# Optimization experiments

Hardware: AMD Instinct MI355X
Metric: run time of the kernel (lower is better)

Reference implementation:

```python
import jax, jax.numpy as jnp
import numpy as np

# Grid / window constants (match init_kwargs)
GX, GY, GZ = 120, 120, 8          # grid_size (x, y, z)
WX, WY, WZ = 8, 8, 2              # window_shape
T = WX * WY * WZ                  # 128 slots per window
C = 48                            # channels after conv_input
H = 8                             # nhead
HD = C // H                       # head dim = 6
FF = 256                          # dim_feedforward
N = 80000                         # occupied voxels
NW = (GX // WX) * (GY // WY) * (GZ // WZ)  # 900 windows (batch_size=1)


def _ln(x, g, b, eps=1e-5):
    mu = jnp.mean(x, -1, keepdims=True)
    var = jnp.mean((x - mu) ** 2, -1, keepdims=True)
    return (x - mu) * jax.lax.rsqrt(var + eps) * g + b


def setup_inputs() -> dict:
    key = jax.random.key(0)
    ks = jax.random.split(key, 16)
    # unique voxel coords (no duplicate (window, slot) pairs)
    rng = np.random.default_rng(0)
    lin = rng.choice(GX * GY * GZ, N, replace=False)
    z = lin // (GX * GY)
    rem = lin % (GX * GY)
    y = rem // GX
    x = rem % GX
    coords = np.stack([np.zeros(N, np.int32), z.astype(np.int32), y.astype(np.int32), x.astype(np.int32)], 1)
    s = 0.02
    inp = {
        "voxel_features": jax.random.normal(ks[0], (N, C), jnp.float32),
        "voxel_coords": jnp.asarray(coords, jnp.int32),
        "Wq": jax.random.normal(ks[1], (C, C)) * s, "bq": jnp.zeros((C,)),
        "Wk": jax.random.normal(ks[2], (C, C)) * s, "bk": jnp.zeros((C,)),
        "Wv": jax.random.normal(ks[3], (C, C)) * s, "bv": jnp.zeros((C,)),
        "Wo": jax.random.normal(ks[4], (C, C)) * s, "bo": jnp.zeros((C,)),
        "ln1_g": jnp.ones((C,)), "ln1_b": jnp.zeros((C,)),
        "W1": jax.random.normal(ks[5], (C, FF)) * s, "b1": jnp.zeros((FF,)),
        "W2": jax.random.normal(ks[6], (FF, C)) * s, "b2": jnp.zeros((C,)),
        "ln2_g": jnp.ones((C,)), "ln2_b": jnp.zeros((C,)),
    }
    return inp


def reference(voxel_features, voxel_coords, Wq, bq, Wk, bk, Wv, bv, Wo, bo,
              ln1_g, ln1_b, W1, b1, W2, b2, ln2_g, ln2_b):
    b = voxel_coords[:, 0]
    z, y, x = voxel_coords[:, 1], voxel_coords[:, 2], voxel_coords[:, 3]
    # window id and in-window slot (unique per voxel)
    win = ((b * (GZ // WZ) + z // WZ) * (GY // WY) + y // WY) * (GX // WX) + x // WX
    slot = (z % WZ) * (WY * WX) + (y % WY) * WX + (x % WX)
    # scatter to padded window buffers  [NW, T, C]
    buf = jnp.zeros((NW, T, C), voxel_features.dtype).at[win, slot].set(voxel_features)
    valid = jnp.zeros((NW, T), bool).at[win, slot].set(True)
    # multi-head self-attention within each window
    q = (buf @ Wq + bq).reshape(NW, T, H, HD)
    k = (buf @ Wk + bk).reshape(NW, T, H, HD)
    v = (buf @ Wv + bv).reshape(NW, T, H, HD)
    scores = jnp.einsum("nqhd,nkhd->nhqk", q, k) / jnp.sqrt(jnp.asarray(HD, buf.dtype))
    scores = jnp.where(valid[:, None, None, :], scores, jnp.asarray(-1e9, buf.dtype))
    attn = jax.nn.softmax(scores, axis=-1)
    ctx = jnp.einsum("nhqk,nkhd->nqhd", attn, v).reshape(NW, T, C)
    ctx = ctx @ Wo + bo
    h = _ln(buf + ctx, ln1_g, ln1_b)                  # post-norm residual 1
    ff = jax.nn.relu(h @ W1 + b1) @ W2 + b2           # FFN
    h = _ln(h + ff, ln2_g, ln2_b)                     # post-norm residual 2
    # scatter back to sparse voxel list  [N, C]
    return h[win, slot]
```

## Files before the change

### kernel.cpp

```cpp
#include <hip/hip_runtime.h>
#include <hip/hip_bf16.h>

constexpr int kGX = 120, kGY = 120, kGZ = 8;
constexpr int kWX = 8, kWY = 8, kWZ = 2;
constexpr int kT  = 128;
constexpr int kC  = 48;
constexpr int kFF = 256;
constexpr int kNW = (kGX/kWX)*(kGY/kWY)*(kGZ/kWZ);
constexpr int kN  = 80000;

constexpr int BQ = 9216,  BK = 9264,  BV = 9312,  BO = 9360;
constexpr int G1 = 9408,  B1L = 9456, G2 = 9504,  B2L = 9552;
constexpr int B1F = 21888;
constexpr int B2F = 34432;
constexpr int WTOT = 34480;

constexpr size_t alup(size_t x) { return ((x + 255) / 256) * 256; }
constexpr size_t SLOT_OFF = alup((size_t)WTOT * 4);
constexpr size_t WQT_OFF  = alup(SLOT_OFF + (size_t)kNW * kT * 4);
constexpr size_t WKT_OFF  = WQT_OFF + 4608;
constexpr size_t WVT_OFF  = WKT_OFF + 4608;
constexpr size_t WOT_OFF  = WVT_OFF + 4608;
constexpr size_t W1TB_OFF = alup(WOT_OFF + 4608);
constexpr size_t W2TB_OFF = alup(W1TB_OFF + (size_t)kFF * kC * 2);
constexpr size_t P0       = alup(W2TB_OFF + (size_t)kC * kFF * 2);
constexpr size_t RSZ      = (size_t)kN * kC * 2;
constexpr size_t QS_OFF   = P0;
constexpr size_t KB_OFF   = P0 + RSZ;
constexpr size_t VB_OFF   = P0 + 2*RSZ;
constexpr size_t CTX_OFF  = P0 + 3*RSZ;
constexpr size_t H_OFF    = alup(P0 + 4*RSZ);

typedef short  bf16x8 __attribute__((ext_vector_type(8)));
typedef float  f32x4  __attribute__((ext_vector_type(4)));
typedef float  f32x2  __attribute__((ext_vector_type(2)));

#if __has_builtin(__builtin_amdgcn_exp2f)
#define EXP2F(x) __builtin_amdgcn_exp2f(x)
#else
#define EXP2F(x) exp2f(x)
#endif

__device__ __forceinline__ float bf2f(unsigned int bits16) {
  return __uint_as_float(bits16 << 16);
}
__device__ __forceinline__ unsigned short f2bf(float f) {
  unsigned int u = __float_as_uint(f);
  u += 0x7fffu + ((u >> 16) & 1u);
  return (unsigned short)(u >> 16);
}
__device__ __forceinline__ f32x2 mkf2(float a, float b) {
  f32x2 r; r.x = a; r.y = b; return r;
}
__device__ __forceinline__ int get_isbf(const unsigned int* g1) {
  return (*g1 != 0x3F800000u) ? 1 : 0;
}

struct ConvArgs {
  const void* src[16];
  void*       dst[16];
  int rows[16];
  int cols[16];
  int obf[16];
};

__global__ void k_prep(ConvArgs a, const unsigned int* __restrict__ g1,
                       const int* __restrict__ coords, int* __restrict__ sm) {
  if (blockIdx.x < 16) {
    const int isbf = get_isbf(g1);
    const int s = blockIdx.x;
    const int R = a.rows[s], C = a.cols[s];
    const int n = R * C;
    const int ob = a.obf[s];
    for (int i = threadIdx.x; i < n; i += blockDim.x) {
      float v = isbf ? bf2f(((const unsigned short*)a.src[s])[i])
                     : ((const float*)a.src[s])[i];
      int oi = i;
      if (C > 1) { int r = i / C, c = i - r * C; oi = c * R + r; }
      if (ob) ((unsigned short*)a.dst[s])[oi] = f2bf(v);
      else    ((float*)a.dst[s])[oi] = v;
    }
  } else {
    int v = (blockIdx.x - 16) * blockDim.x + threadIdx.x;
    if (v >= kN) return;
    int z = coords[v*4 + 1], y = coords[v*4 + 2], x = coords[v*4 + 3];
    int win  = ((z/kWZ) * (kGY/kWY) + y/kWY) * (kGX/kWX) + x/kWX;
    int slot = (z%kWZ) * (kWY*kWX) + (y%kWY) * kWX + (x%kWX);
    sm[win*kT + slot] = v;
  }
}

__global__ __attribute__((amdgpu_waves_per_eu(2, 4))) __launch_bounds__(256)
void k_qkv3(const void* __restrict__ feats_raw,
            const unsigned int* __restrict__ g1,
            const unsigned short* __restrict__ wqt,
            const unsigned short* __restrict__ wkt,
            const unsigned short* __restrict__ wvt,
            const float* __restrict__ w,
            unsigned short* __restrict__ Qs,
            unsigned short* __restrict__ Kb,
            unsigned short* __restrict__ Vb)
{
  __shared__ unsigned short At[128*72];
  __shared__ unsigned short Bt[3][48*72];

  const int isbf = get_isbf(g1);
  const int tid = threadIdx.x, bm = blockIdx.x;

  if (isbf) {
    const uint4* asrc = (const uint4*)((const unsigned short*)feats_raw +
                                       (size_t)bm * 128 * kC);
    #pragma unroll
    for (int i = 0; i < 3; ++i) {
      int cid = tid + 256*i;
      int row = cid / 6, ch = cid - row*6;
      *(uint4*)((char*)At + row*144 + ch*16) = asrc[row*6 + ch];
    }
  } else {
    const float4* asrc = (const float4*)((const float*)feats_raw +
                                         (size_t)bm * 128 * kC);
    #pragma unroll
    for (int i = 0; i < 3; ++i) {
      int cid = tid + 256*i;
      int row = cid / 6, ch = cid - row*6;
      float4 f0 = asrc[row*12 + ch*2], f1 = asrc[row*12 + ch*2 + 1];
      uint4 o;
      o.x = (unsigned int)f2bf(f0.x) | ((unsigned int)f2bf(f0.y) << 16);
      o.y = (unsigned int)f2bf(f0.z) | ((unsigned int)f2bf(f0.w) << 16);
      o.z = (unsigned int)f2bf(f1.x) | ((unsigned int)f2bf(f1.y) << 16);
      o.w = (unsigned int)f2bf(f1.z) | ((unsigned int)f2bf(f1.w) << 16);
      *(uint4*)((char*)At + row*144 + ch*16) = o;
    }
  }
  {
    int row = tid >> 1, ch = 6 + (tid & 1);
    *(uint4*)((char*)At + row*144 + ch*16) = make_uint4(0,0,0,0);
  }
  #pragma unroll
  for (int y = 0; y < 3; ++y) {
    const uint4* bsrc = (const uint4*)((y == 0) ? wqt : (y == 1) ? wkt : wvt);
    #pragma unroll
    for (int i = 0; i < 2; ++i) {
      int cid = tid + 256*i;
      if (cid < 288) {
        int row = cid / 6, ch = cid - row*6;
        *(uint4*)((char*)Bt[y] + row*144 + ch*16) = bsrc[row*6 + ch];
      }
    }
    if (tid < 96) {
      int row = tid >> 1, ch = 6 + (tid & 1);
      *(uint4*)((char*)Bt[y] + row*144 + ch*16) = make_uint4(0,0,0,0);
    }
  }
  __syncthreads();

  const int lane = tid & 63, wv = tid >> 6;
  const int moff = wv * 32;
  const int lr = lane & 15, lc = lane >> 4;

  #pragma unroll
  for (int y = 0; y < 3; ++y) {
    unsigned short* dst = (y == 0) ? Qs : (y == 1) ? Kb : Vb;
    const float* bias = w + ((y == 0) ? BQ : (y == 1) ? BK : BV);
    const float scl = (y == 0) ? 0.5889777931f : 1.0f;

    f32x4 acc[2][3] = {};
    #pragma unroll
    for (int ks = 0; ks < 2; ++ks) {
      bf16x8 a[2], b[3];
      #pragma unroll
      for (int m = 0; m < 2; ++m)
        a[m] = *(const bf16x8*)((const char*)At +
                (moff + m*16 + lr)*144 + lc*16 + ks*64);
      #pragma unroll
      for (int n = 0; n < 3; ++n)
        b[n] = *(const bf16x8*)((const char*)Bt[y] +
                (n*16 + lr)*144 + lc*16 + ks*64);
      #pragma unroll
      for (int m = 0; m < 2; ++m)
        #pragma unroll
        for (int n = 0; n < 3; ++n)
          acc[m][n] = __builtin_amdgcn_mfma_f32_16x16x32_bf16(
                          a[m], b[n], acc[m][n], 0, 0, 0);
    }
    #pragma unroll
    for (int n = 0; n < 3; ++n) {
      const int col = n*16 + lr;
      const float bv = bias[col];
      #pragma unroll
      for (int m = 0; m < 2; ++m) {
        const int row0 = bm*128 + moff + m*16 + lc*4;
        #pragma unroll
        for (int r = 0; r < 4; ++r)
          dst[(size_t)(row0 + r) * kC + col] = f2bf((acc[m][n][r] + bv) * scl);
      }
    }
  }
}

#define ATTN_KEY(KK, ACC, LP) {                                               \
    const float4* kp_ = (const float4*)(KfF + (size_t)(KK)*48 + q*12);        \
    const float4* vp_ = (const float4*)(VfF + (size_t)(KK)*48 + q*12);        \
    float4 k0_ = kp_[0], k1_ = kp_[1], k2_ = kp_[2];                          \
    f32x2 p0_ = qp[0] * mkf2(k0_.x, k0_.y);                                   \
    p0_ += qp[1] * mkf2(k0_.z, k0_.w);                                        \
    p0_ += qp[2] * mkf2(k1_.x, k1_.y);                                        \
    f32x2 p1_ = qp[3] * mkf2(k1_.z, k1_.w);                                   \
    p1_ += qp[4] * mkf2(k2_.x, k2_.y);                                        \
    p1_ += qp[5] * mkf2(k2_.z, k2_.w);                                        \
    float w0_ = EXP2F(p0_.x + p0_.y);                                         \
    float w1_ = EXP2F(p1_.x + p1_.y);                                         \
    float4 v0_ = vp_[0], v1_ = vp_[1], v2_ = vp_[2];                          \
    LP += mkf2(w0_, w1_);                                                     \
    f32x2 w0p_ = mkf2(w0_, w0_), w1p_ = mkf2(w1_, w1_);                       \
    ACC[0] += w0p_ * mkf2(v0_.x, v0_.y);                                      \
    ACC[1] += w0p_ * mkf2(v0_.z, v0_.w);                                      \
    ACC[2] += w0p_ * mkf2(v1_.x, v1_.y);                                      \
    ACC[3] += w1p_ * mkf2(v1_.z, v1_.w);                                      \
    ACC[4] += w1p_ * mkf2(v2_.x, v2_.y);                                      \
    ACC[5] += w1p_ * mkf2(v2_.z, v2_.w);                                      \
  }

__global__ __attribute__((amdgpu_waves_per_eu(2, 6))) __launch_bounds__(512)
void k_attn2f(const unsigned short* __restrict__ Qs,
              const unsigned short* __restrict__ Kb,
              const unsigned short* __restrict__ Vb,
              const int* __restrict__ sm,
              unsigned short* __restrict__ ctxb)
{
  __shared__ __align__(16) float KfF[kT*kC];
  __shared__ __align__(16) float VfF[kT*kC];
  __shared__ int posmap[kT];
  __shared__ unsigned long long wmask[2];

  const int win = blockIdx.x;
  const int tid = threadIdx.x;
  const int q   = tid >> 7;
  const int t   = tid & 127;
  const int vid = sm[win*kT + t];
  const bool valid = vid >= 0;

  unsigned long long bm = __ballot(valid);
  if (tid < 128 && (tid & 63) == 0) wmask[tid >> 6] = bm;
  __syncthreads();

  const int cnt0 = __popcll(wmask[0]);
  const int nk   = cnt0 + __popcll(wmask[1]);
  if (tid < 128) {
    int pos = -1;
    if (valid) {
      unsigned long long lanemask = (1ull << (t & 63)) - 1ull;
      pos = ((t >> 6) ? cnt0 : 0) + __popcll(wmask[t >> 6] & lanemask);
    }
    posmap[t] = pos;
  }
  __syncthreads();

  #pragma unroll
  for (int i = 0; i < 3; ++i) {
    int cid = tid + 512*i;
    int mat = cid / 768;
    int r   = cid - mat*768;
    int slot = r / 6, ch = r - slot*6;
    int p = posmap[slot];
    if (p >= 0) {
      int svid = sm[win*kT + slot];
      const unsigned short* src = mat ? Vb : Kb;
      uint4 u = *(const uint4*)(src + (size_t)svid * kC + ch*8);
      float* d = (mat ? VfF : KfF) + p*48 + ch*8;
      float4 f0, f1;
      f0.x = bf2f(u.x & 0xffffu); f0.y = bf2f(u.x >> 16);
      f0.z = bf2f(u.y & 0xffffu); f0.w = bf2f(u.y >> 16);
      f1.x = bf2f(u.z & 0xffffu); f1.y = bf2f(u.z >> 16);
      f1.z = bf2f(u.w & 0xffffu); f1.w = bf2f(u.w >> 16);
      *(float4*)d = f0;
      *(float4*)(d + 4) = f1;
    }
  }
  __syncthreads();

  f32x2 qp[6];
  #pragma unroll
  for (int j = 0; j < 6; ++j) qp[j] = mkf2(0.f, 0.f);
  if (valid) {
    const unsigned short* qptr = Qs + (size_t)vid * kC + q*12;
    uint2 q0 = *(const uint2*)(qptr);
    uint2 q1 = *(const uint2*)(qptr + 4);
    uint2 q2 = *(const uint2*)(qptr + 8);
    unsigned int qw[6] = {q0.x, q0.y, q1.x, q1.y, q2.x, q2.y};
    #pragma unroll
    for (int j = 0; j < 6; ++j)
      qp[j] = mkf2(bf2f(qw[j] & 0xffffu), bf2f(qw[j] >> 16));
  }

  f32x2 accA[6], accB[6];
  f32x2 lA = mkf2(0.f, 0.f), lB = mkf2(0.f, 0.f);
  #pragma unroll
  for (int j = 0; j < 6; ++j) { accA[j] = mkf2(0.f, 0.f); accB[j] = mkf2(0.f, 0.f); }

  int i = 0;
  for (; i + 2 <= nk; i += 2) {
    ATTN_KEY(i,     accA, lA);
    ATTN_KEY(i + 1, accB, lB);
  }
  if (i < nk) {
    ATTN_KEY(i, accA, lA);
  }
  lA += lB;
  #pragma unroll
  for (int j = 0; j < 6; ++j) accA[j] += accB[j];

  if (valid) {
    float i0 = (lA.x > 0.f) ? (1.f / lA.x) : 0.f;
    float i1 = (lA.y > 0.f) ? (1.f / lA.y) : 0.f;
    unsigned int pw[6];
    #pragma unroll
    for (int j = 0; j < 6; ++j) {
      float sc = (j < 3) ? i0 : i1;
      pw[j] = (unsigned int)f2bf(accA[j].x * sc) |
              ((unsigned int)f2bf(accA[j].y * sc) << 16);
    }
    unsigned short* cp = ctxb + (size_t)vid * kC + q*12;
    *(uint2*)(cp)     = make_uint2(pw[0], pw[1]);
    *(uint2*)(cp + 4) = make_uint2(pw[2], pw[3]);
    *(uint2*)(cp + 8) = make_uint2(pw[4], pw[5]);
  }
}

__global__ __attribute__((amdgpu_waves_per_eu(2, 4))) __launch_bounds__(256)
void k_woln1(const unsigned short* __restrict__ ctxb,
             const unsigned short* __restrict__ wot,
             const void* __restrict__ feats_raw,
             const unsigned int* __restrict__ g1,
             const float* __restrict__ w,
             unsigned short* __restrict__ hbuf)
{
  __shared__ unsigned short At[128*72];
  __shared__ unsigned short Bt[48*72];
  __shared__ float Cf[128][49];

  const int isbf = get_isbf(g1);
  const int tid = threadIdx.x, bm = blockIdx.x;

  const uint4* asrc = (const uint4*)(ctxb + (size_t)bm * 128 * kC);
  #pragma unroll
  for (int i = 0; i < 3; ++i) {
    int cid = tid + 256*i;
    int row = cid / 6, ch = cid - row*6;
    *(uint4*)((char*)At + row*144 + ch*16) = asrc[row*6 + ch];
  }
  {
    int row = tid >> 1, ch = 6 + (tid & 1);
    *(uint4*)((char*)At + row*144 + ch*16) = make_uint4(0,0,0,0);
  }
  {
    const uint4* bsrc = (const uint4*)wot;
    #pragma unroll
    for (int i = 0; i < 2; ++i) {
      int cid = tid + 256*i;
      if (cid < 288) {
        int row = cid / 6, ch = cid - row*6;
        *(uint4*)((char*)Bt + row*144 + ch*16) = bsrc[row*6 + ch];
      }
    }
    if (tid < 96) {
      int row = tid >> 1, ch = 6 + (tid & 1);
      *(uint4*)((char*)Bt + row*144 + ch*16) = make_uint4(0,0,0,0);
    }
  }
  __syncthreads();

  const int lane = tid & 63, wv = tid >> 6;
  const int moff = wv * 32;
  const int lr = lane & 15, lc = lane >> 4;

  f32x4 acc[2][3] = {};
  #pragma unroll
  for (int ks = 0; ks < 2; ++ks) {
    bf16x8 a[2], b[3];
    #pragma unroll
    for (int m = 0; m < 2; ++m)
      a[m] = *(const bf16x8*)((const char*)At +
              (moff + m*16 + lr)*144 + lc*16 + ks*64);
    #pragma unroll
    for (int n = 0; n < 3; ++n)
      b[n] = *(const bf16x8*)((const char*)Bt +
              (n*16 + lr)*144 + lc*16 + ks*64);
    #pragma unroll
    for (int m = 0; m < 2; ++m)
      #pragma unroll
      for (int n = 0; n < 3; ++n)
        acc[m][n] = __builtin_amdgcn_mfma_f32_16x16x32_bf16(
                        a[m], b[n], acc[m][n], 0, 0, 0);
  }

  #pragma unroll
  for (int n = 0; n < 3; ++n) {
    const int col = n*16 + lr;
    const float bo = w[BO + col];
    #pragma unroll
    for (int m = 0; m < 2; ++m) {
      const int row0 = moff + m*16 + lc*4;
      #pragma unroll
      for (int r = 0; r < 4; ++r)
        Cf[row0 + r][col] = acc[m][n][r] + bo;
    }
  }
  __syncthreads();

  if (tid < 128) {
    const size_t gvox = (size_t)bm * 128 + tid;
    float xrow[kC];
    if (isbf) {
      const uint4* xp = (const uint4*)((const unsigned short*)feats_raw +
                                       gvox * kC);
      #pragma unroll
      for (int i = 0; i < 6; ++i) {
        uint4 u = xp[i];
        unsigned int uu[4] = {u.x, u.y, u.z, u.w};
        #pragma unroll
        for (int j = 0; j < 4; ++j) {
          xrow[i*8 + j*2 + 0] = bf2f(uu[j] & 0xffffu);
          xrow[i*8 + j*2 + 1] = bf2f(uu[j] >> 16);
        }
      }
    } else {
      const float4* xp = (const float4*)((const float*)feats_raw + gvox * kC);
      #pragma unroll
      for (int i = 0; i < 12; ++i) {
        float4 u = xp[i];
        xrow[i*4+0] = u.x; xrow[i*4+1] = u.y;
        xrow[i*4+2] = u.z; xrow[i*4+3] = u.w;
      }
    }
    float val[kC];
    float mu = 0.f;
    #pragma unroll
    for (int c = 0; c < kC; ++c) {
      float v = Cf[tid][c] + xrow[c];
      val[c] = v;
      mu += v;
    }
    mu *= (1.f / kC);
    float var = 0.f;
    #pragma unroll
    for (int c = 0; c < kC; ++c) { float d = val[c] - mu; var += d * d; }
    var *= (1.f / kC);
    float rs = rsqrtf(var + 1e-5f);

    unsigned int pk[kC/2];
    #pragma unroll
    for (int cp = 0; cp < kC/2; ++cp) {
      float h0 = (val[2*cp]   - mu) * rs * w[G1 + 2*cp]   + w[B1L + 2*cp];
      float h1 = (val[2*cp+1] - mu) * rs * w[G1 + 2*cp+1] + w[B1L + 2*cp+1];
      pk[cp] = (unsigned int)f2bf(h0) | ((unsigned int)f2bf(h1) << 16);
    }
    uint4* op = (uint4*)(hbuf + gvox * kC);
    #pragma unroll
    for (int i = 0; i < 6; ++i)
      op[i] = make_uint4(pk[i*4+0], pk[i*4+1], pk[i*4+2], pk[i*4+3]);
  }
}

__global__ __attribute__((amdgpu_waves_per_eu(2, 2))) __launch_bounds__(256)
void k_ffln(const unsigned short* __restrict__ hb,
            const unsigned short* __restrict__ w1tb,
            const unsigned short* __restrict__ w2tb,
            const float* __restrict__ w,
            void* __restrict__ out_raw,
            const unsigned int* __restrict__ g1)
{
  __shared__ __align__(16) char L[71424];
  unsigned short* W2t = (unsigned short*)(L + 18432);
  unsigned short* Bt  = (unsigned short*)(L + 43776);
  unsigned short* Ut  = (unsigned short*)(L + 52992);
  float* Cf = (float*)(L + 43776);

  const int isbf = get_isbf(g1);
  const int tid = threadIdx.x, bm = blockIdx.x;

  const uint4* hsrc = (const uint4*)(hb + (size_t)bm * 128 * kC);
  #pragma unroll
  for (int i = 0; i < 3; ++i) {
    int cid = tid + 256*i;
    int row = cid / 6, ch = cid - row*6;
    *(uint4*)(L + row*144 + ch*16) = hsrc[row*6 + ch];
  }
  {
    int row = tid >> 1, ch = 6 + (tid & 1);
    *(uint4*)(L + row*144 + ch*16) = make_uint4(0,0,0,0);
  }
  {
    const uint4* wsrc = (const uint4*)w2tb;
    #pragma unroll
    for (int i = 0; i < 6; ++i) {
      int cid = tid + 256*i;
      int row = cid >> 5, ch = cid & 31;
      *(uint4*)((char*)W2t + row*528 + ch*16) = wsrc[row*32 + ch];
    }
  }

  const int lane = tid & 63, wv = tid >> 6;
  const int moff = wv * 32;
  const int lr = lane & 15, lc = lane >> 4;

  f32x4 acc2[2][3] = {};

  for (int qn = 0; qn < 4; ++qn) {
    __syncthreads();
    {
      const uint4* bsrc = (const uint4*)(w1tb + (size_t)qn * 64 * kC);
      #pragma unroll
      for (int i = 0; i < 2; ++i) {
        int cid = tid + 256*i;
        if (cid < 384) {
          int row = cid / 6, ch = cid - row*6;
          *(uint4*)((char*)Bt + row*144 + ch*16) = bsrc[row*6 + ch];
        }
      }
      if (tid < 128) {
        int row = tid >> 1, ch = 6 + (tid & 1);
        *(uint4*)((char*)Bt + row*144 + ch*16) = make_uint4(0,0,0,0);
      }
    }
    __syncthreads();

    f32x4 acc1[2][4] = {};
    #pragma unroll
    for (int ks = 0; ks < 2; ++ks) {
      bf16x8 a[2], b[4];
      #pragma unroll
      for (int m = 0; m < 2; ++m)
        a[m] = *(const bf16x8*)(L + (moff + m*16 + lr)*144 + lc*16 + ks*64);
      #pragma unroll
      for (int n = 0; n < 4; ++n)
        b[n] = *(const bf16x8*)((const char*)Bt +
                (n*16 + lr)*144 + lc*16 + ks*64);
      #pragma unroll
      for (int m = 0; m < 2; ++m)
        #pragma unroll
        for (int n = 0; n < 4; ++n)
          acc1[m][n] = __builtin_amdgcn_mfma_f32_16x16x32_bf16(
                           a[m], b[n], acc1[m][n], 0, 0, 0);
    }

    #pragma unroll
    for (int n = 0; n < 4; ++n) {
      const float bias = w[B1F + qn*64 + n*16 + lr];
      #pragma unroll
      for (int m = 0; m < 2; ++m) {
        #pragma unroll
        for (int r = 0; r < 4; ++r) {
          float v = fmaxf(acc1[m][n][r] + bias, 0.f);
          Ut[(moff + m*16 + lc*4 + r)*72 + n*16 + lr] = f2bf(v);
        }
      }
    }

    #pragma unroll
    for (int ks = 0; ks < 2; ++ks) {
      bf16x8 a[2], b[3];
      #pragma unroll
      for (int m = 0; m < 2; ++m)
        a[m] = *(const bf16x8*)((const char*)Ut +
                (moff + m*16 + lr)*144 + lc*16 + ks*64);
      #pragma unroll
      for (int n = 0; n < 3; ++n)
        b[n] = *(const bf16x8*)((const char*)W2t +
                (n*16 + lr)*528 + qn*128 + ks*64 + lc*16);
      #pragma unroll
      for (int m = 0; m < 2; ++m)
        #pragma unroll
        for (int n = 0; n < 3; ++n)
          acc2[m][n] = __builtin_amdgcn_mfma_f32_16x16x32_bf16(
                           a[m], b[n], acc2[m][n], 0, 0, 0);
    }
  }

  __syncthreads();

  #pragma unroll
  for (int n = 0; n < 3; ++n) {
    const int col = n*16 + lr;
    const float b2v = w[B2F + col];
    #pragma unroll
    for (int m = 0; m < 2; ++m) {
      const int row0 = moff + m*16 + lc*4;
      #pragma unroll
      for (int r = 0; r < 4; ++r)
        Cf[(row0 + r)*49 + col] = acc2[m][n][r] + b2v;
    }
  }
  __syncthreads();

  if (tid < 128) {
    const size_t gvox = (size_t)bm * 128 + tid;
    const uint4* hp = (const uint4*)(hb + gvox * kC);
    float val[kC];
    float mu = 0.f;
    #pragma unroll
    for (int i = 0; i < 6; ++i) {
      uint4 u = hp[i];
      unsigned int uu[4] = {u.x, u.y, u.z, u.w};
      #pragma unroll
      for (int j = 0; j < 4; ++j) {
        float v0 = Cf[tid*49 + i*8 + j*2 + 0] + bf2f(uu[j] & 0xffffu);
        float v1 = Cf[tid*49 + i*8 + j*2 + 1] + bf2f(uu[j] >> 16);
        val[i*8 + j*2 + 0] = v0;
        val[i*8 + j*2 + 1] = v1;
        mu += v0 + v1;
      }
    }
    mu *= (1.f / kC);
    float var = 0.f;
    #pragma unroll
    for (int c = 0; c < kC; ++c) { float d = val[c] - mu; var += d * d; }
    var *= (1.f / kC);
    float rs = rsqrtf(var + 1e-5f);

    float ov[kC];
    #pragma unroll
    for (int c = 0; c < kC; ++c)
      ov[c] = (val[c] - mu) * rs * w[G2 + c] + w[B2L + c];

    if (isbf) {
      unsigned int pk[kC/2];
      #pragma unroll
      for (int c = 0; c < kC; c += 2)
        pk[c/2] = (unsigned int)f2bf(ov[c]) | ((unsigned int)f2bf(ov[c+1]) << 16);
      uint4* op = (uint4*)((unsigned short*)out_raw + gvox * kC);
      #pragma unroll
      for (int i = 0; i < 6; ++i)
        op[i] = make_uint4(pk[i*4+0], pk[i*4+1], pk[i*4+2], pk[i*4+3]);
    } else {
      float4* op = (float4*)((float*)out_raw + gvox * kC);
      #pragma unroll
      for (int i = 0; i < 12; ++i)
        op[i] = make_float4(ov[i*4+0], ov[i*4+1], ov[i*4+2], ov[i*4+3]);
    }
  }
}

extern "C" void kernel_launch(void* const* d_in, const int* in_sizes, int n_in,
                              void* d_out, int out_size, void* d_ws, size_t ws_size,
                              hipStream_t stream) {
  const void* feats = d_in[0];
  const int* coords = (const int*)d_in[1];
  const unsigned int* g1 = (const unsigned int*)d_in[10];
  char* ws = (char*)d_ws;
  float* wbuf = (float*)d_ws;
  int* sm   = (int*)(ws + SLOT_OFF);
  unsigned short* wqt  = (unsigned short*)(ws + WQT_OFF);
  unsigned short* wkt  = (unsigned short*)(ws + WKT_OFF);
  unsigned short* wvt  = (unsigned short*)(ws + WVT_OFF);
  unsigned short* wot  = (unsigned short*)(ws + WOT_OFF);
  unsigned short* w1tb = (unsigned short*)(ws + W1TB_OFF);
  unsigned short* w2tb = (unsigned short*)(ws + W2TB_OFF);
  unsigned short* Qs   = (unsigned short*)(ws + QS_OFF);
  unsigned short* Kb   = (unsigned short*)(ws + KB_OFF);
  unsigned short* Vb   = (unsigned short*)(ws + VB_OFF);
  unsigned short* ctxb = (unsigned short*)(ws + CTX_OFF);
  unsigned short* hbuf = (unsigned short*)(ws + H_OFF);

  ConvArgs ca;
  const int srcIdx[16] = {2,4,6,8, 3,5,7,9, 10,11,16,17, 12,13,14,15};
  void* dsts[16] = {
    wqt, wkt, wvt, wot,
    wbuf+BQ, wbuf+BK, wbuf+BV, wbuf+BO,
    wbuf+G1, wbuf+B1L, wbuf+G2, wbuf+B2L,
    w1tb, wbuf+B1F, w2tb, wbuf+B2F };
  const int rows[16] = {48,48,48,48, 48,48,48,48, 48,48,48,48, 48,256,256,48};
  const int cols[16] = {48,48,48,48, 1,1,1,1, 1,1,1,1, 256,1,48,1};
  const int obfs[16] = {1,1,1,1, 0,0,0,0, 0,0,0,0, 1,0,1,0};
  for (int i = 0; i < 16; ++i) {
    ca.src[i]  = d_in[srcIdx[i]];
    ca.dst[i]  = dsts[i];
    ca.rows[i] = rows[i];
    ca.cols[i] = cols[i];
    ca.obf[i]  = obfs[i];
  }

  hipMemsetAsync(sm, 0xFF, (size_t)kNW * kT * 4, stream);
  hipLaunchKernelGGL(k_prep, dim3(16 + (kN + 255)/256), dim3(256), 0, stream,
                     ca, g1, coords, sm);
  hipLaunchKernelGGL(k_qkv3, dim3(kN/128), dim3(256), 0, stream,
                     feats, g1, wqt, wkt, wvt, wbuf, Qs, Kb, Vb);
  hipLaunchKernelGGL(k_attn2f, dim3(kNW), dim3(512), 0, stream,
                     Qs, Kb, Vb, sm, ctxb);
  hipLaunchKernelGGL(k_woln1, dim3(kN/128), dim3(256), 0, stream,
                     ctxb, wot, feats, g1, wbuf, hbuf);
  hipLaunchKernelGGL(k_ffln, dim3(kN/128), dim3(256), 0, stream,
                     hbuf, w1tb, w2tb, wbuf, d_out, g1);
}
```

Measured before the change: 117.4 us.

## Process two queries per thread in attention to reuse K/V shared loads

The attention kernel now launches 256 threads per window instead of 512, and each thread handles two query slots (lane and lane+64) for a quarter of the heads. Each K/V row read from shared memory feeds both queries, halving LDS traffic per unit of work. In exchange it uses more registers per thread, runs fewer threads per block, and drops the two-key unrolling, which may cut latency hiding.

```diff
diff --git a/kernel.cpp b/kernel.cpp
--- a/kernel.cpp
+++ b/kernel.cpp
@@ -198,31 +198,8 @@
   }
 }
 
-#define ATTN_KEY(KK, ACC, LP) {                                               \
-    const float4* kp_ = (const float4*)(KfF + (size_t)(KK)*48 + q*12);        \
-    const float4* vp_ = (const float4*)(VfF + (size_t)(KK)*48 + q*12);        \
-    float4 k0_ = kp_[0], k1_ = kp_[1], k2_ = kp_[2];                          \
-    f32x2 p0_ = qp[0] * mkf2(k0_.x, k0_.y);                                   \
-    p0_ += qp[1] * mkf2(k0_.z, k0_.w);                                        \
-    p0_ += qp[2] * mkf2(k1_.x, k1_.y);                                        \
-    f32x2 p1_ = qp[3] * mkf2(k1_.z, k1_.w);                                   \
-    p1_ += qp[4] * mkf2(k2_.x, k2_.y);                                        \
-    p1_ += qp[5] * mkf2(k2_.z, k2_.w);                                        \
-    float w0_ = EXP2F(p0_.x + p0_.y);                                         \
-    float w1_ = EXP2F(p1_.x + p1_.y);                                         \
-    float4 v0_ = vp_[0], v1_ = vp_[1], v2_ = vp_[2];                          \
-    LP += mkf2(w0_, w1_);                                                     \
-    f32x2 w0p_ = mkf2(w0_, w0_), w1p_ = mkf2(w1_, w1_);                       \
-    ACC[0] += w0p_ * mkf2(v0_.x, v0_.y);                                      \
-    ACC[1] += w0p_ * mkf2(v0_.z, v0_.w);                                      \
-    ACC[2] += w0p_ * mkf2(v1_.x, v1_.y);                                      \
-    ACC[3] += w1p_ * mkf2(v1_.z, v1_.w);                                      \
-    ACC[4] += w1p_ * mkf2(v2_.x, v2_.y);                                      \
-    ACC[5] += w1p_ * mkf2(v2_.z, v2_.w);                                      \
-  }
-
-__global__ __attribute__((amdgpu_waves_per_eu(2, 6))) __launch_bounds__(512)
-void k_attn2f(const unsigned short* __restrict__ Qs,
+__global__ __attribute__((amdgpu_waves_per_eu(2, 4))) __launch_bounds__(256)
+void k_attn2h(const unsigned short* __restrict__ Qs,
               const unsigned short* __restrict__ Kb,
               const unsigned short* __restrict__ Vb,
               const int* __restrict__ sm,
@@ -233,32 +210,33 @@
   __shared__ int posmap[kT];
   __shared__ unsigned long long wmask[2];
 
-  const int win = blockIdx.x;
-  const int tid = threadIdx.x;
-  const int q   = tid >> 7;
-  const int t   = tid & 127;
-  const int vid = sm[win*kT + t];
-  const bool valid = vid >= 0;
-
-  unsigned long long bm = __ballot(valid);
-  if (tid < 128 && (tid & 63) == 0) wmask[tid >> 6] = bm;
+  const int win  = blockIdx.x;
+  const int tid  = threadIdx.x;
+  const int q    = tid >> 6;
+  const int lane = tid & 63;
+
+  if (tid < 128) {
+    bool val = sm[win*kT + tid] >= 0;
+    unsigned long long bm = __ballot(val);
+    if ((tid & 63) == 0) wmask[tid >> 6] = bm;
+  }
   __syncthreads();
 
   const int cnt0 = __popcll(wmask[0]);
   const int nk   = cnt0 + __popcll(wmask[1]);
   if (tid < 128) {
     int pos = -1;
-    if (valid) {
-      unsigned long long lanemask = (1ull << (t & 63)) - 1ull;
-      pos = ((t >> 6) ? cnt0 : 0) + __popcll(wmask[t >> 6] & lanemask);
-    }
-    posmap[t] = pos;
+    if (sm[win*kT + tid] >= 0) {
+      unsigned long long lanemask = (1ull << (tid & 63)) - 1ull;
+      pos = ((tid >> 6) ? cnt0 : 0) + __popcll(wmask[tid >> 6] & lanemask);
+    }
+    posmap[tid] = pos;
   }
   __syncthreads();
 
   #pragma unroll
-  for (int i = 0; i < 3; ++i) {
-    int cid = tid + 512*i;
+  for (int i = 0; i < 6; ++i) {
+    int cid = tid + 256*i;
     int mat = cid / 768;
     int r   = cid - mat*768;
     int slot = r / 6, ch = r - slot*6;
@@ -279,18 +257,32 @@
   }
   __syncthreads();
 
-  f32x2 qp[6];
-  #pragma unroll
-  for (int j = 0; j < 6; ++j) qp[j] = mkf2(0.f, 0.f);
-  if (valid) {
-    const unsigned short* qptr = Qs + (size_t)vid * kC + q*12;
+  const int vidA = sm[win*kT + lane];
+  const int vidB = sm[win*kT + 64 + lane];
+  const bool validA = vidA >= 0, validB = vidB >= 0;
+
+  f32x2 qpA[6], qpB[6];
+  #pragma unroll
+  for (int j = 0; j < 6; ++j) { qpA[j] = mkf2(0.f, 0.f); qpB[j] = mkf2(0.f, 0.f); }
+  if (validA) {
+    const unsigned short* qptr = Qs + (size_t)vidA * kC + q*12;
     uint2 q0 = *(const uint2*)(qptr);
     uint2 q1 = *(const uint2*)(qptr + 4);
     uint2 q2 = *(const uint2*)(qptr + 8);
     unsigned int qw[6] = {q0.x, q0.y, q1.x, q1.y, q2.x, q2.y};
     #pragma unroll
     for (int j = 0; j < 6; ++j)
-      qp[j] = mkf2(bf2f(qw[j] & 0xffffu), bf2f(qw[j] >> 16));
+      qpA[j] = mkf2(bf2f(qw[j] & 0xffffu), bf2f(qw[j] >> 16));
+  }
+  if (validB) {
+    const unsigned short* qptr = Qs + (size_t)vidB * kC + q*12;
+    uint2 q0 = *(const uint2*)(qptr);
+    uint2 q1 = *(const uint2*)(qptr + 4);
+    uint2 q2 = *(const uint2*)(qptr + 8);
+    unsigned int qw[6] = {q0.x, q0.y, q1.x, q1.y, q2.x, q2.y};
+    #pragma unroll
+    for (int j = 0; j < 6; ++j)
+      qpB[j] = mkf2(bf2f(qw[j] & 0xffffu), bf2f(qw[j] >> 16));
   }
 
   f32x2 accA[6], accB[6];
@@ -298,19 +290,49 @@
   #pragma unroll
   for (int j = 0; j < 6; ++j) { accA[j] = mkf2(0.f, 0.f); accB[j] = mkf2(0.f, 0.f); }
 
-  int i = 0;
-  for (; i + 2 <= nk; i += 2) {
-    ATTN_KEY(i,     accA, lA);
-    ATTN_KEY(i + 1, accB, lB);
-  }
-  if (i < nk) {
-    ATTN_KEY(i, accA, lA);
-  }
-  lA += lB;
-  #pragma unroll
-  for (int j = 0; j < 6; ++j) accA[j] += accB[j];
-
-  if (valid) {
+  const float* kbase = KfF + q*12;
+  const float* vbase = VfF + q*12;
+  for (int kk = 0; kk < nk; ++kk) {
+    const float4* kp = (const float4*)(kbase + (size_t)kk*48);
+    const float4* vp = (const float4*)(vbase + (size_t)kk*48);
+    float4 k0 = kp[0], k1 = kp[1], k2 = kp[2];
+    float4 v0 = vp[0], v1 = vp[1], v2 = vp[2];
+    f32x2 pA0 = qpA[0] * mkf2(k0.x, k0.y);
+    pA0 += qpA[1] * mkf2(k0.z, k0.w);
+    pA0 += qpA[2] * mkf2(k1.x, k1.y);
+    f32x2 pA1 = qpA[3] * mkf2(k1.z, k1.w);
+    pA1 += qpA[4] * mkf2(k2.x, k2.y);
+    pA1 += qpA[5] * mkf2(k2.z, k2.w);
+    float wA0 = EXP2F(pA0.x + pA0.y);
+    float wA1 = EXP2F(pA1.x + pA1.y);
+    f32x2 pB0 = qpB[0] * mkf2(k0.x, k0.y);
+    pB0 += qpB[1] * mkf2(k0.z, k0.w);
+    pB0 += qpB[2] * mkf2(k1.x, k1.y);
+    f32x2 pB1 = qpB[3] * mkf2(k1.z, k1.w);
+    pB1 += qpB[4] * mkf2(k2.x, k2.y);
+    pB1 += qpB[5] * mkf2(k2.z, k2.w);
+    float wB0 = EXP2F(pB0.x + pB0.y);
+    float wB1 = EXP2F(pB1.x + pB1.y);
+
+    lA += mkf2(wA0, wA1);
+    lB += mkf2(wB0, wB1);
+    f32x2 wA0p = mkf2(wA0, wA0), wA1p = mkf2(wA1, wA1);
+    f32x2 wB0p = mkf2(wB0, wB0), wB1p = mkf2(wB1, wB1);
+    accA[0] += wA0p * mkf2(v0.x, v0.y);
+    accA[1] += wA0p * mkf2(v0.z, v0.w);
+    accA[2] += wA0p * mkf2(v1.x, v1.y);
+    accA[3] += wA1p * mkf2(v1.z, v1.w);
+    accA[4] += wA1p * mkf2(v2.x, v2.y);
+    accA[5] += wA1p * mkf2(v2.z, v2.w);
+    accB[0] += wB0p * mkf2(v0.x, v0.y);
+    accB[1] += wB0p * mkf2(v0.z, v0.w);
+    accB[2] += wB0p * mkf2(v1.x, v1.y);
+    accB[3] += wB1p * mkf2(v1.z, v1.w);
+    accB[4] += wB1p * mkf2(v2.x, v2.y);
+    accB[5] += wB1p * mkf2(v2.z, v2.w);
+  }
+
+  if (validA) {
     float i0 = (lA.x > 0.f) ? (1.f / lA.x) : 0.f;
     float i1 = (lA.y > 0.f) ? (1.f / lA.y) : 0.f;
     unsigned int pw[6];
@@ -320,7 +342,22 @@
       pw[j] = (unsigned int)f2bf(accA[j].x * sc) |
               ((unsigned int)f2bf(accA[j].y * sc) << 16);
     }
-    unsigned short* cp = ctxb + (size_t)vid * kC + q*12;
+    unsigned short* cp = ctxb + (size_t)vidA * kC + q*12;
+    *(uint2*)(cp)     = make_uint2(pw[0], pw[1]);
+    *(uint2*)(cp + 4) = make_uint2(pw[2], pw[3]);
+    *(uint2*)(cp + 8) = make_uint2(pw[4], pw[5]);
+  }
+  if (validB) {
+    float i0 = (lB.x > 0.f) ? (1.f / lB.x) : 0.f;
+    float i1 = (lB.y > 0.f) ? (1.f / lB.y) : 0.f;
+    unsigned int pw[6];
+    #pragma unroll
+    for (int j = 0; j < 6; ++j) {
+      float sc = (j < 3) ? i0 : i1;
+      pw[j] = (unsigned int)f2bf(accB[j].x * sc) |
+              ((unsigned int)f2bf(accB[j].y * sc) << 16);
+    }
+    unsigned short* cp = ctxb + (size_t)vidB * kC + q*12;
     *(uint2*)(cp)     = make_uint2(pw[0], pw[1]);
     *(uint2*)(cp + 4) = make_uint2(pw[2], pw[3]);
     *(uint2*)(cp + 8) = make_uint2(pw[4], pw[5]);
@@ -685,7 +722,7 @@
                      ca, g1, coords, sm);
   hipLaunchKernelGGL(k_qkv3, dim3(kN/128), dim3(256), 0, stream,
                      feats, g1, wqt, wkt, wvt, wbuf, Qs, Kb, Vb);
-  hipLaunchKernelGGL(k_attn2f, dim3(kNW), dim3(512), 0, stream,
+  hipLaunchKernelGGL(k_attn2h, dim3(kNW), dim3(256), 0, stream,
                      Qs, Kb, Vb, sm, ctxb);
   hipLaunchKernelGGL(k_woln1, dim3(kN/128), dim3(256), 0, stream,
                      ctxb, wot, feats, g1, wbuf, hbuf);
```

Result: faster. 114.7 us (-2.3%).
